# Optimization experiments

Hardware: AMD Instinct MI355X
Metric: run time of the kernel (lower is better)

## Reference

```python
import jax, jax.numpy as jnp
import numpy as np

B, CIN, COUT, T, H, W = 8, 512, 256, 8, 16, 16


def conv1x1(x, w, b):
    # 1x1x1 Conv3d == per-position channel GEMM. x:[B,Ci,T,H,W], w:[Co,Ci], b:[Co]
    return jnp.einsum('bcthw,oc->bothw', x, w) + b[None, :, None, None, None]


def setup_inputs() -> dict:
    key = jax.random.key(0)
    ks = jax.random.split(key, 12)
    s_in = 1.0 / np.sqrt(CIN)
    s_out = 1.0 / np.sqrt(COUT)
    return {
        'x': jax.random.normal(ks[0], (B, CIN, T, H, W), jnp.float32),
        'query': jax.random.normal(ks[1], (B, CIN, T, H, W), jnp.float32),
        'key_w': jax.random.uniform(ks[2], (COUT, CIN), jnp.float32, -s_in, s_in),
        'key_b': jax.random.uniform(ks[3], (COUT,), jnp.float32, -s_in, s_in),
        'val_w': jax.random.uniform(ks[4], (COUT, CIN), jnp.float32, -s_in, s_in),
        'val_b': jax.random.uniform(ks[5], (COUT,), jnp.float32, -s_in, s_in),
        'query_w': jax.random.uniform(ks[6], (COUT, CIN), jnp.float32, -s_in, s_in),
        'query_b': jax.random.uniform(ks[7], (COUT,), jnp.float32, -s_in, s_in),
        'up_w': jax.random.uniform(ks[8], (CIN, COUT), jnp.float32, -s_out, s_out),
        'up_b': jax.random.uniform(ks[9], (CIN,), jnp.float32, -s_out, s_out),
        'scaling': jnp.asarray(1.0, jnp.float32),
    }


def reference(x, query, key_w, key_b, val_w, val_b, query_w, query_b, up_w, up_b, scaling):
    b, ci, t, h, w = x.shape
    n = t * h * w
    co = key_w.shape[0]
    k = conv1x1(x, key_w, key_b).reshape(b, co, n)          # [B,Co,N]
    q = conv1x1(query, query_w, query_b).reshape(b, co, n)  # [B,Co,N]
    v = conv1x1(x, val_w, val_b).reshape(b, co, n)          # [B,Co,N]
    # attention = (key^T @ query) / sqrt(Co)  -> [B,N,N], softmax over last dim
    attn = jnp.einsum('bcn,bcm->bnm', k, q) / jnp.sqrt(jnp.asarray(co, x.dtype))
    attn = jax.nn.softmax(attn, axis=-1)
    out = jnp.einsum('bnm,bcm->bnc', attn, v)               # [B,N,Co]
    # faithful to torch .view: raw-memory reshape of [B,N,Co] -> [B,Co,T,H,W]
    out = out.reshape(b, co, t, h, w)
    out = conv1x1(out, up_w, up_b)                          # [B,Ci,T,H,W]
    return x + out * scaling
```

## Files before the change

kernel.cpp:

```cpp
#include <hip/hip_runtime.h>
#include <hip/hip_fp8.h>
#include <math.h>

#define NB 8
#define CI 512
#define CO 256
#define NN 2048
#define SCALE 0.0625f
#define SPLIT 4

typedef __bf16 v8bf __attribute__((ext_vector_type(8)));
typedef __bf16 v4bf __attribute__((ext_vector_type(4)));
typedef float  f32x4  __attribute__((ext_vector_type(4)));
typedef float  f32x16 __attribute__((ext_vector_type(16)));
typedef unsigned char u8;
typedef long i64t;

static __device__ __forceinline__ u8 to_fp8(float x) {
    __hip_fp8_e4m3 t(x);
    return (u8)t.__x;
}

static __device__ __forceinline__ i64t pack64(unsigned lo, unsigned hi) {
    return (i64t)(((unsigned long long)hi << 32) | (unsigned long long)lo);
}

__global__ __launch_bounds__(256, 2)
void proj3_kernel(const float* __restrict__ x, const float* __restrict__ query,
                  const float* __restrict__ wk, const float* __restrict__ bk,
                  const float* __restrict__ wv, const float* __restrict__ bv,
                  const float* __restrict__ wq, const float* __restrict__ bq,
                  u8* __restrict__ outK, u8* __restrict__ outV, u8* __restrict__ outQ)
{
    const int b = blockIdx.z, n0 = blockIdx.x * 128, co0 = blockIdx.y * 64;
    const int tid = threadIdx.x;
    const int wave = tid >> 6, lane = tid & 63;
    const int l16 = lane & 15, quad = lane >> 4;
    const int wn = wave & 1, wc = wave >> 1;

    __shared__ __bf16 Xt[128][40];
    __shared__ __bf16 Qt[128][40];
    __shared__ __bf16 Wks[64][40];
    __shared__ __bf16 Wvs[64][40];
    __shared__ __bf16 Wqs[64][40];

    const float* xb = x + (size_t)b * CI * NN;
    const float* qb = query + (size_t)b * CI * NN;

    f32x4 acck[4][2], accv[2][4], accq[4][2];
    #pragma unroll
    for (int i = 0; i < 4; ++i)
        #pragma unroll
        for (int j = 0; j < 2; ++j) {
            acck[i][j] = f32x4{0,0,0,0}; accv[j][i] = f32x4{0,0,0,0};
            accq[i][j] = f32x4{0,0,0,0};
        }

    const int xn = tid & 127;
    const int xc = tid >> 7;

    for (int k0 = 0; k0 < CI; k0 += 32) {
        #pragma unroll
        for (int g = 0; g < 2; ++g) {
            int cg = xc + g * 2;
            v8bf z, w;
            #pragma unroll
            for (int j = 0; j < 8; ++j) {
                z[j] = (__bf16)xb[(size_t)(k0 + cg * 8 + j) * NN + n0 + xn];
                w[j] = (__bf16)qb[(size_t)(k0 + cg * 8 + j) * NN + n0 + xn];
            }
            *(v8bf*)&Xt[xn][cg * 8] = z;
            *(v8bf*)&Qt[xn][cg * 8] = w;
        }
        #pragma unroll
        for (int g = 0; g < 2; ++g) {
            int f = tid + 256 * g;
            int co = f >> 3, cq = f & 7;
            float4 a = *(const float4*)(wk + (size_t)(co0 + co) * CI + k0 + cq * 4);
            float4 c = *(const float4*)(wv + (size_t)(co0 + co) * CI + k0 + cq * 4);
            float4 d = *(const float4*)(wq + (size_t)(co0 + co) * CI + k0 + cq * 4);
            *(v4bf*)&Wks[co][cq * 4] = v4bf{(__bf16)a.x, (__bf16)a.y, (__bf16)a.z, (__bf16)a.w};
            *(v4bf*)&Wvs[co][cq * 4] = v4bf{(__bf16)c.x, (__bf16)c.y, (__bf16)c.z, (__bf16)c.w};
            *(v4bf*)&Wqs[co][cq * 4] = v4bf{(__bf16)d.x, (__bf16)d.y, (__bf16)d.z, (__bf16)d.w};
        }
        __syncthreads();
        v8bf ax[4], aqx[4], bkf[2], bqf[2];
        #pragma unroll
        for (int i = 0; i < 4; ++i) {
            ax[i]  = *(const v8bf*)&Xt[wn * 64 + i * 16 + l16][quad * 8];
            aqx[i] = *(const v8bf*)&Qt[wn * 64 + i * 16 + l16][quad * 8];
        }
        #pragma unroll
        for (int j = 0; j < 2; ++j) {
            bkf[j] = *(const v8bf*)&Wks[wc * 32 + j * 16 + l16][quad * 8];
            bqf[j] = *(const v8bf*)&Wqs[wc * 32 + j * 16 + l16][quad * 8];
        }
        #pragma unroll
        for (int i = 0; i < 4; ++i)
            #pragma unroll
            for (int j = 0; j < 2; ++j) {
                acck[i][j] = __builtin_amdgcn_mfma_f32_16x16x32_bf16(ax[i],  bkf[j], acck[i][j], 0, 0, 0);
                accq[i][j] = __builtin_amdgcn_mfma_f32_16x16x32_bf16(aqx[i], bqf[j], accq[i][j], 0, 0, 0);
            }
        {
            v8bf avf[2];
            #pragma unroll
            for (int j = 0; j < 2; ++j) avf[j] = *(const v8bf*)&Wvs[wc * 32 + j * 16 + l16][quad * 8];
            #pragma unroll
            for (int j = 0; j < 2; ++j)
                #pragma unroll
                for (int i = 0; i < 4; ++i)
                    accv[j][i] = __builtin_amdgcn_mfma_f32_16x16x32_bf16(avf[j], ax[i], accv[j][i], 0, 0, 0);
        }
        __syncthreads();
    }
    #pragma unroll
    for (int i = 0; i < 4; ++i) {
        int n = n0 + wn * 64 + i * 16 + quad * 4;
        #pragma unroll
        for (int j = 0; j < 2; ++j) {
            int co = co0 + wc * 32 + j * 16 + l16;
            float bkk = bk[co], bqq = bq[co];
            u8* dk = outK + ((size_t)b * NN + n) * CO + co;
            u8* dq = outQ + ((size_t)b * NN + n) * CO + co;
            #pragma unroll
            for (int r = 0; r < 4; ++r) {
                dk[(size_t)r * CO] = to_fp8(acck[i][j][r] + bkk);
                dq[(size_t)r * CO] = to_fp8(accq[i][j][r] + bqq);
            }
        }
    }
    #pragma unroll
    for (int j = 0; j < 2; ++j) {
        int co = co0 + wc * 32 + j * 16 + quad * 4;
        #pragma unroll
        for (int r = 0; r < 4; ++r) {
            float bvv = bv[co + r];
            #pragma unroll
            for (int i = 0; i < 4; ++i) {
                int n = n0 + wn * 64 + i * 16 + l16;
                outV[((size_t)b * CO + co + r) * NN + n] = to_fp8(accv[j][i][r] + bvv);
            }
        }
    }
}

__global__ __launch_bounds__(256, 2)
void attn_kernel(const u8* __restrict__ kT, const u8* __restrict__ qT,
                 const u8* __restrict__ vT2, __bf16* __restrict__ Opart,
                 float* __restrict__ lbuf)
{
    const int b = blockIdx.z, part = blockIdx.y, n0 = blockIdx.x * 128;
    const int tid = threadIdx.x;
    const int wave = tid >> 6, lane = tid & 63;
    const int l32 = lane & 31, hs = lane >> 5;

    __shared__ i64t Ks8[64][33];
    __shared__ i64t Vt8[256][9];

    const int start = part * (NN / SPLIT);
    const u8* Ksrc = qT + ((size_t)b * NN + start) * CO;
    const u8* Vsrc = vT2 + (size_t)b * CO * NN + start;

    i64t aq[16];
    {
        const u8* qrow = kT + ((size_t)b * NN + n0 + wave * 32 + l32) * CO + hs * 8;
        #pragma unroll
        for (int s = 0; s < 16; ++s) aq[s] = *(const i64t*)(qrow + s * 16);
    }

    f32x16 acc[8];
    #pragma unroll
    for (int t = 0; t < 8; ++t)
        #pragma unroll
        for (int r = 0; r < 16; ++r) acc[t][r] = 0.f;
    float lp = 0.f;

    int4 kx[4], vx[4];
    #pragma unroll
    for (int r2 = 0; r2 < 4; ++r2) {
        int c = tid + 256 * r2;
        kx[r2] = *(const int4*)(Ksrc + (size_t)(c >> 4) * CO + (c & 15) * 16);
        vx[r2] = *(const int4*)(Vsrc + (size_t)(c >> 2) * NN + (c & 3) * 16);
    }

    for (int it = 0; it < NN / SPLIT / 64; ++it) {
        #pragma unroll
        for (int r2 = 0; r2 < 4; ++r2) {
            int c = tid + 256 * r2;
            i64t* kd = &Ks8[c >> 4][(c & 15) * 2];
            kd[0] = *(const i64t*)&kx[r2].x;
            kd[1] = *(const i64t*)&kx[r2].z;
            i64t* vd = &Vt8[c >> 2][(c & 3) * 2];
            vd[0] = pack64((unsigned)vx[r2].x, (unsigned)vx[r2].z);
            vd[1] = pack64((unsigned)vx[r2].y, (unsigned)vx[r2].w);
        }
        __syncthreads();

        if (it + 1 < NN / SPLIT / 64) {
            const u8* Kit = Ksrc + (size_t)(it + 1) * 64 * CO;
            const u8* Vit = Vsrc + (it + 1) * 64;
            #pragma unroll
            for (int r2 = 0; r2 < 4; ++r2) {
                int c = tid + 256 * r2;
                kx[r2] = *(const int4*)(Kit + (size_t)(c >> 4) * CO + (c & 15) * 16);
                vx[r2] = *(const int4*)(Vit + (size_t)(c >> 2) * NN + (c & 3) * 16);
            }
        }

        int dpk[8];
        #pragma unroll
        for (int sub = 0; sub < 2; ++sub) {
            f32x16 sacc;
            #pragma unroll
            for (int r = 0; r < 16; ++r) sacc[r] = 0.f;
            __builtin_amdgcn_s_setprio(1);
            #pragma unroll
            for (int s = 0; s < 16; ++s) {
                i64t kf = Ks8[sub * 32 + l32][s * 2 + hs];
                sacc = __builtin_amdgcn_mfma_f32_32x32x16_fp8_fp8(kf, aq[s], sacc, 0, 0, 0);
            }
            __builtin_amdgcn_s_setprio(0);
            #pragma unroll
            for (int r = 0; r < 16; ++r) {
                sacc[r] = __expf(sacc[r] * SCALE);
                lp += sacc[r];
            }
            #pragma unroll
            for (int g = 0; g < 4; ++g) {
                int lo = __builtin_amdgcn_cvt_pk_fp8_f32(sacc[4*g+0], sacc[4*g+1], 0, false);
                dpk[sub * 4 + g] = __builtin_amdgcn_cvt_pk_fp8_f32(sacc[4*g+2], sacc[4*g+3], lo, true);
            }
        }
        i64t pa[4];
        #pragma unroll
        for (int c = 0; c < 4; ++c)
            pa[c] = pack64((unsigned)dpk[2 * c], (unsigned)dpk[2 * c + 1]);

        __builtin_amdgcn_s_setprio(1);
        #pragma unroll
        for (int t = 0; t < 8; ++t) {
            #pragma unroll
            for (int c = 0; c < 4; ++c) {
                i64t bvf = Vt8[t * 32 + l32][c * 2 + hs];
                acc[t] = __builtin_amdgcn_mfma_f32_32x32x16_fp8_fp8(pa[c], bvf, acc[t], 0, 0, 0);
            }
        }
        __builtin_amdgcn_s_setprio(0);
        __syncthreads();
    }

    lp += __shfl_xor(lp, 32);
    if (hs == 0)
        lbuf[(size_t)(part * NB + b) * NN + n0 + wave * 32 + l32] = lp;

    const size_t qbase = (size_t)(part * NB + b) * NN + n0 + wave * 32;
    #pragma unroll
    for (int t = 0; t < 8; ++t)
        #pragma unroll
        for (int r = 0; r < 16; ++r) {
            int row = (r & 3) + 8 * (r >> 2) + 4 * hs;
            Opart[(qbase + row) * CO + t * 32 + l32] = (__bf16)acc[t][r];
        }
}

__global__ __launch_bounds__(256)
void merge_kernel(const __bf16* __restrict__ Opart, const float* __restrict__ lbuf,
                  __bf16* __restrict__ ob)
{
    int gid = blockIdx.x * 256 + threadIdx.x;
    int chunk = gid & 31;
    int row = gid >> 5;
    float ls = 0.f;
    #pragma unroll
    for (int p = 0; p < SPLIT; ++p) ls += lbuf[(size_t)p * NB * NN + row];
    float inv = 1.0f / ls;
    float o[8] = {0,0,0,0,0,0,0,0};
    #pragma unroll
    for (int p = 0; p < SPLIT; ++p) {
        v8bf v = *(const v8bf*)(Opart + ((size_t)p * NB * NN + row) * CO + chunk * 8);
        #pragma unroll
        for (int j = 0; j < 8; ++j) o[j] += (float)v[j];
    }
    v8bf res;
    #pragma unroll
    for (int j = 0; j < 8; ++j) res[j] = (__bf16)(o[j] * inv);
    *(v8bf*)(ob + (size_t)row * CO + chunk * 8) = res;
}

__global__ __launch_bounds__(256)
void up_kernel(const __bf16* __restrict__ ob, const float* __restrict__ x,
               const float* __restrict__ w2, const float* __restrict__ b2,
               const float* __restrict__ scaling, float* __restrict__ out)
{
    const int b = blockIdx.z, n0 = blockIdx.x * 128, ci0 = blockIdx.y * 128;
    const int tid = threadIdx.x;
    const int wave = tid >> 6, lane = tid & 63;
    const int l16 = lane & 15, quad = lane >> 4;
    const int wn = wave & 1, wci = wave >> 1;

    __shared__ __bf16 Zt[128][40];
    __shared__ __bf16 Wt[128][40];

    const __bf16* obb = ob + (size_t)b * CO * NN;

    f32x4 acc[4][4];
    #pragma unroll
    for (int i = 0; i < 4; ++i)
        #pragma unroll
        for (int j = 0; j < 4; ++j) acc[i][j] = f32x4{0,0,0,0};

    const int zm = tid & 15;
    const int zcv = tid >> 4;
    const int zsw = 8 * (zm & 3);

    for (int k0 = 0; k0 < CO; k0 += 32) {
        #pragma unroll
        for (int u = 0; u < 2; ++u) {
            const int cv = zcv + 16 * u;
            v8bf z = *(const v8bf*)(obb + (size_t)(k0 + cv) * NN + n0 + zm * 8);
            const int col = cv ^ zsw;
            #pragma unroll
            for (int i = 0; i < 8; ++i)
                Zt[zm * 8 + i][col] = z[i];
        }
        #pragma unroll
        for (int g = 0; g < 4; ++g) {
            int f = tid + 256 * g;
            int ci = f >> 3, cq = f & 7;
            float4 v = *(const float4*)(w2 + (size_t)(ci0 + ci) * CO + k0 + cq * 4);
            *(v4bf*)&Wt[ci][cq * 4] = v4bf{(__bf16)v.x, (__bf16)v.y, (__bf16)v.z, (__bf16)v.w};
        }
        __syncthreads();
        v8bf aw[4], bz[4];
        #pragma unroll
        for (int i = 0; i < 4; ++i) aw[i] = *(const v8bf*)&Wt[wci * 64 + i * 16 + l16][quad * 8];
        #pragma unroll
        for (int j = 0; j < 4; ++j) {
            const int row = wn * 64 + j * 16 + l16;
            const int col = (quad ^ ((row >> 3) & 3)) * 8;
            bz[j] = *(const v8bf*)&Zt[row][col];
        }
        #pragma unroll
        for (int i = 0; i < 4; ++i)
            #pragma unroll
            for (int j = 0; j < 4; ++j)
                acc[i][j] = __builtin_amdgcn_mfma_f32_16x16x32_bf16(aw[i], bz[j], acc[i][j], 0, 0, 0);
        __syncthreads();
    }
    float sc = scaling[0];
    #pragma unroll
    for (int i = 0; i < 4; ++i) {
        int ci = ci0 + wci * 64 + i * 16 + quad * 4;
        #pragma unroll
        for (int r = 0; r < 4; ++r) {
            float bvv = b2[ci + r];
            #pragma unroll
            for (int j = 0; j < 4; ++j) {
                int n = n0 + wn * 64 + j * 16 + l16;
                size_t gi = ((size_t)b * CI + ci + r) * NN + n;
                out[gi] = x[gi] + sc * (acc[i][j][r] + bvv);
            }
        }
    }
}

extern "C" void kernel_launch(void* const* d_in, const int* in_sizes, int n_in,
                              void* d_out, int out_size, void* d_ws, size_t ws_size,
                              hipStream_t stream)
{
    (void)in_sizes; (void)n_in; (void)out_size; (void)ws_size;
    const float* x       = (const float*)d_in[0];
    const float* query   = (const float*)d_in[1];
    const float* key_w   = (const float*)d_in[2];
    const float* key_b   = (const float*)d_in[3];
    const float* val_w   = (const float*)d_in[4];
    const float* val_b   = (const float*)d_in[5];
    const float* query_w = (const float*)d_in[6];
    const float* query_b = (const float*)d_in[7];
    const float* up_w    = (const float*)d_in[8];
    const float* up_b    = (const float*)d_in[9];
    const float* scaling = (const float*)d_in[10];
    float* out = (float*)d_out;

    const size_t TEN = (size_t)NB * NN * CO;
    u8* kT  = (u8*)d_ws;
    u8* qT  = kT + TEN;
    u8* vT2 = qT + TEN;
    __bf16* ob    = (__bf16*)(vT2 + TEN);
    __bf16* Opart = ob + TEN;
    float*  lbuf  = (float*)(Opart + (size_t)SPLIT * TEN);

    dim3 blk(256);
    proj3_kernel<<<dim3(NN / 128, CO / 64, NB), blk, 0, stream>>>(
        x, query, key_w, key_b, val_w, val_b, query_w, query_b, kT, vT2, qT);
    attn_kernel<<<dim3(NN / 128, SPLIT, NB), blk, 0, stream>>>(kT, qT, vT2, Opart, lbuf);
    merge_kernel<<<dim3((NB * NN * CO / 8) / 256), blk, 0, stream>>>(Opart, lbuf, ob);
    up_kernel<<<dim3(NN / 128, CI / 128, NB), blk, 0, stream>>>(ob, x, up_w, up_b, scaling, out);
}
```

Before: 206.8 us.

## Fuse split-softmax merge into up-projection kernel and drop intermediate buffer

Removes the separate merge kernel and instead has the up-projection kernel sum the SPLIT partial outputs and normalise by the summed softmax denominators while loading its tile. This saves a kernel launch and the write/read round trip of the merged bf16 buffer. In exchange, every ci-block of the up kernel re-reads and re-reduces all partial outputs, multiplying global/L2 traffic for Opart.

Result: no change. 205.1 us, median of 2 (-0.9%).

```diff
diff --git a/kernel.cpp b/kernel.cpp
--- a/kernel.cpp
+++ b/kernel.cpp
@@ -265,31 +265,8 @@
 }
 
 __global__ __launch_bounds__(256)
-void merge_kernel(const __bf16* __restrict__ Opart, const float* __restrict__ lbuf,
-                  __bf16* __restrict__ ob)
-{
-    int gid = blockIdx.x * 256 + threadIdx.x;
-    int chunk = gid & 31;
-    int row = gid >> 5;
-    float ls = 0.f;
-    #pragma unroll
-    for (int p = 0; p < SPLIT; ++p) ls += lbuf[(size_t)p * NB * NN + row];
-    float inv = 1.0f / ls;
-    float o[8] = {0,0,0,0,0,0,0,0};
-    #pragma unroll
-    for (int p = 0; p < SPLIT; ++p) {
-        v8bf v = *(const v8bf*)(Opart + ((size_t)p * NB * NN + row) * CO + chunk * 8);
-        #pragma unroll
-        for (int j = 0; j < 8; ++j) o[j] += (float)v[j];
-    }
-    v8bf res;
-    #pragma unroll
-    for (int j = 0; j < 8; ++j) res[j] = (__bf16)(o[j] * inv);
-    *(v8bf*)(ob + (size_t)row * CO + chunk * 8) = res;
-}
-
-__global__ __launch_bounds__(256)
-void up_kernel(const __bf16* __restrict__ ob, const float* __restrict__ x,
+void up_kernel(const __bf16* __restrict__ Opart, const float* __restrict__ lbuf,
+               const float* __restrict__ x,
                const float* __restrict__ w2, const float* __restrict__ b2,
                const float* __restrict__ scaling, float* __restrict__ out)
 {
@@ -301,8 +278,20 @@
 
     __shared__ __bf16 Zt[128][40];
     __shared__ __bf16 Wt[128][40];
-
-    const __bf16* obb = ob + (size_t)b * CO * NN;
+    __shared__ float invl[256];
+
+    const size_t PSTRIDE = (size_t)NB * NN * CO;
+    const __bf16* Opb = Opart + (size_t)b * NN * CO;
+
+    {
+        const int norig = tid * 8 + (n0 >> 8);
+        float ls = 0.f;
+        #pragma unroll
+        for (int p = 0; p < SPLIT; ++p)
+            ls += lbuf[(size_t)(p * NB + b) * NN + norig];
+        invl[tid] = 1.0f / ls;
+    }
+    __syncthreads();
 
     f32x4 acc[4][4];
     #pragma unroll
@@ -318,11 +307,19 @@
         #pragma unroll
         for (int u = 0; u < 2; ++u) {
             const int cv = zcv + 16 * u;
-            v8bf z = *(const v8bf*)(obb + (size_t)(k0 + cv) * NN + n0 + zm * 8);
+            const size_t fbase = (size_t)(k0 + cv) * NN + n0 + zm * 8;
+            float s[8] = {0,0,0,0,0,0,0,0};
+            #pragma unroll
+            for (int p = 0; p < SPLIT; ++p) {
+                v8bf v = *(const v8bf*)(Opb + (size_t)p * PSTRIDE + fbase);
+                #pragma unroll
+                for (int j = 0; j < 8; ++j) s[j] += (float)v[j];
+            }
+            const float il = invl[k0 + cv];
             const int col = cv ^ zsw;
             #pragma unroll
             for (int i = 0; i < 8; ++i)
-                Zt[zm * 8 + i][col] = z[i];
+                Zt[zm * 8 + i][col] = (__bf16)(s[i] * il);
         }
         #pragma unroll
         for (int g = 0; g < 4; ++g) {
@@ -387,14 +384,13 @@
     u8* kT  = (u8*)d_ws;
     u8* qT  = kT + TEN;
     u8* vT2 = qT + TEN;
-    __bf16* ob    = (__bf16*)(vT2 + TEN);
-    __bf16* Opart = ob + TEN;
+    __bf16* Opart = (__bf16*)(vT2 + TEN);
     float*  lbuf  = (float*)(Opart + (size_t)SPLIT * TEN);
 
     dim3 blk(256);
     proj3_kernel<<<dim3(NN / 128, CO / 64, NB), blk, 0, stream>>>(
         x, query, key_w, key_b, val_w, val_b, query_w, query_b, kT, vT2, qT);
     attn_kernel<<<dim3(NN / 128, SPLIT, NB), blk, 0, stream>>>(kT, qT, vT2, Opart, lbuf);
-    merge_kernel<<<dim3((NB * NN * CO / 8) / 256), blk, 0, stream>>>(Opart, lbuf, ob);
-    up_kernel<<<dim3(NN / 128, CI / 128, NB), blk, 0, stream>>>(ob, x, up_w, up_b, scaling, out);
-}
+    up_kernel<<<dim3(NN / 128, CI / 128, NB), blk, 0, stream>>>(
+        Opart, lbuf, x, up_w, up_b, scaling, out);
+}
```
